# Performance work log

Hardware: AMD Instinct MI355X
Metric: run time of the kernel (lower is better)

Reference implementation:

```python
import jax, jax.numpy as jnp
import numpy as np

N, E, IN, D, G, C = 100000, 3200000, 128, 512, 64, 10
EPS = 1e-5

def _bn(x, g, b):
    # training-mode BatchNorm1d: batch statistics, biased variance
    m = jnp.mean(x, axis=0)
    v = jnp.var(x, axis=0)
    return (x - m) * jax.lax.rsqrt(v + EPS) * g + b

def _prelu(x, a):
    return jnp.where(x >= 0, x, a * x)

def setup_inputs() -> dict:
    key = jax.random.key(0)
    ks = jax.random.split(key, 16)
    def w(k, shape):
        fan_in = shape[0]
        s = 1.0 / np.sqrt(fan_in)
        return jax.random.uniform(k, shape, jnp.float32, -s, s)
    inp = {
        'x': jax.random.normal(ks[0], (N, IN), jnp.float32),
        'edge_index': jax.random.randint(ks[1], (2, E), 0, N),
        'batch': jnp.sort(jax.random.randint(ks[2], (N,), 0, G)),
        'bn1_g': jnp.ones((IN,), jnp.float32), 'bn1_b': jnp.zeros((IN,), jnp.float32),
        'w0': w(ks[3], (IN, D)), 'b0': jnp.zeros((D,), jnp.float32),
        'w1': w(ks[4], (D, D)), 'bb1': jnp.zeros((D,), jnp.float32),
        'w2': w(ks[5], (D, D)), 'bb2': jnp.zeros((D,), jnp.float32),
        'w3': w(ks[6], (D, D)), 'bb3': jnp.zeros((D,), jnp.float32),
        'bn3_g': jnp.ones((D,), jnp.float32), 'bn3_b': jnp.zeros((D,), jnp.float32),
        'a3': jnp.array([0.25], jnp.float32),
        'fc1_w': w(ks[7], (D, D)), 'fc1_b': jnp.zeros((D,), jnp.float32),
        'fc2_w': w(ks[8], (D, D // 2)), 'fc2_b': jnp.zeros((D // 2,), jnp.float32),
        'fc3_w': w(ks[9], (D // 2, C)), 'fc3_b': jnp.zeros((C,), jnp.float32),
    }
    return inp

def reference(x, edge_index, batch, bn1_g, bn1_b, w0, b0, w1, bb1, w2, bb2, w3, bb3,
              bn3_g, bn3_b, a3, fc1_w, fc1_b, fc2_w, fc2_b, fc3_w, fc3_b):
    # ChebConv with K=1 reduces to a plain linear layer (T_0(L)x = x); edge_index unused.
    h = _bn(x, bn1_g, bn1_b)
    h = jax.nn.relu(h @ w0 + b0)
    for w_, b_ in ((w1, bb1), (w2, bb2), (w3, bb3)):
        h = jax.nn.relu(h @ w_ + b_)
        h = _bn(h, bn3_g, bn3_b)   # same bn3 module reused each layer
    # global_add_pool: segment-sum of node features per graph
    h = jax.ops.segment_sum(h, batch, num_segments=G)
    h = _prelu(h @ fc1_w + fc1_b, a3)
    h = jax.nn.sigmoid(h @ fc2_w + fc2_b)
    return h @ fc3_w + fc3_b
```

## Files before the change

kernel.cpp:

```cpp
#include <hip/hip_runtime.h>
#include <math.h>

#define NN 100000
#define INF 128
#define DD  512
#define GG  64
#define CC  10

typedef __bf16 bf16;
typedef __bf16 bf16x8 __attribute__((ext_vector_type(8)));
typedef __bf16 bf16x4 __attribute__((ext_vector_type(4)));
typedef float  f32x4  __attribute__((ext_vector_type(4)));
typedef unsigned int u32x4 __attribute__((ext_vector_type(4)));


__global__ void zero_k(float* __restrict__ p, int n) {
    int i = blockIdx.x * blockDim.x + threadIdx.x;
    if (i < n) p[i] = 0.0f;
}

__global__ void bounds_k(const int* __restrict__ batch, int* __restrict__ starts) {
    int g = threadIdx.x;
    if (g <= GG) {
        int lo = 0, hi = NN;
        while (lo < hi) {
            int mid = (lo + hi) >> 1;
            if (batch[mid] < g) lo = mid + 1; else hi = mid;
        }
        starts[g] = lo;
    }
}

__global__ __launch_bounds__(256)
void colstats_cvt(const float* __restrict__ x, bf16* __restrict__ xb,
                  float* __restrict__ stats) {
    __shared__ float rs[4][128], rq[4][128];
    int t = threadIdx.x;
    int w = t >> 6, l = t & 63;
    int rg = t >> 5;
    int cq = t & 31;
    float s0 = 0, s1 = 0, s2 = 0, s3 = 0, q0 = 0, q1 = 0, q2 = 0, q3 = 0;
    for (int row = blockIdx.x * 8 + rg; row < NN; row += gridDim.x * 8) {
        float4 v = *(const float4*)&x[(size_t)row * INF + cq * 4];
        bf16x4 o; o[0] = (bf16)v.x; o[1] = (bf16)v.y; o[2] = (bf16)v.z; o[3] = (bf16)v.w;
        *(bf16x4*)&xb[(size_t)row * INF + cq * 4] = o;
        s0 += v.x; q0 += v.x * v.x;
        s1 += v.y; q1 += v.y * v.y;
        s2 += v.z; q2 += v.z * v.z;
        s3 += v.w; q3 += v.w * v.w;
    }
    s0 += __shfl_xor(s0, 32); s1 += __shfl_xor(s1, 32);
    s2 += __shfl_xor(s2, 32); s3 += __shfl_xor(s3, 32);
    q0 += __shfl_xor(q0, 32); q1 += __shfl_xor(q1, 32);
    q2 += __shfl_xor(q2, 32); q3 += __shfl_xor(q3, 32);
    if (l < 32) {
        rs[w][cq * 4 + 0] = s0; rs[w][cq * 4 + 1] = s1;
        rs[w][cq * 4 + 2] = s2; rs[w][cq * 4 + 3] = s3;
        rq[w][cq * 4 + 0] = q0; rq[w][cq * 4 + 1] = q1;
        rq[w][cq * 4 + 2] = q2; rq[w][cq * 4 + 3] = q3;
    }
    __syncthreads();
    if (t < 128) {
        atomicAdd(&stats[t],       rs[0][t] + rs[1][t] + rs[2][t] + rs[3][t]);
        atomicAdd(&stats[INF + t], rq[0][t] + rq[1][t] + rq[2][t] + rq[3][t]);
    }
}

__global__ void prep_st(const float* __restrict__ stats, int K,
                        const float* __restrict__ gamma, const float* __restrict__ beta,
                        float* __restrict__ s, float* __restrict__ t) {
    int j = blockIdx.x * blockDim.x + threadIdx.x;
    if (j < K) {
        const float invN = 1.0f / (float)NN;
        float mean = stats[j] * invN;
        float var  = stats[K + j] * invN - mean * mean;
        float sv   = gamma[j] * rsqrtf(var + 1e-5f);
        s[j] = sv;
        t[j] = beta[j] - mean * sv;
    }
}

__global__ __launch_bounds__(256)
void fold_wt(const float* __restrict__ s, const float* __restrict__ W,
             bf16* __restrict__ Wt, int K) {
    __shared__ float tile[64][68];
    __shared__ float sarr[64];
    int j0 = blockIdx.x * 64, k0 = blockIdx.y * 64;
    int t = threadIdx.x;
    if (t < 64) sarr[t] = s ? s[k0 + t] : 1.0f;
    int kk = t >> 2, jq = t & 3;
#pragma unroll
    for (int i = 0; i < 4; i++) {
        float4 v = *(const float4*)&W[(size_t)(k0 + kk) * DD + j0 + jq * 16 + i * 4];
        *(float4*)&tile[kk][jq * 16 + i * 4] = v;
    }
    __syncthreads();
    int jj = t >> 2, kq = t & 3;
    bf16 ov[16];
#pragma unroll
    for (int i = 0; i < 16; i++)
        ov[i] = (bf16)(tile[kq * 16 + i][jj] * sarr[kq * 16 + i]);
    bf16* dst = &Wt[(size_t)(j0 + jj) * K + k0 + kq * 16];
    *(u32x4*)dst       = *(u32x4*)&ov[0];
    *(u32x4*)(dst + 8) = *(u32x4*)&ov[8];
}

__global__ __launch_bounds__(256)
void fold_b(const float* __restrict__ tv, const float* __restrict__ W,
            const float* __restrict__ b, float* __restrict__ bp, int K) {
    __shared__ float red[4][64];
    int jj = threadIdx.x & 63, kr = threadIdx.x >> 6;
    int j = blockIdx.x * 64 + jj;
    float acc = 0.f;
    for (int k = kr; k < K; k += 4)
        acc += tv[k] * W[(size_t)k * DD + j];
    red[kr][jj] = acc;
    __syncthreads();
    if (kr == 0) bp[j] = b[j] + red[0][jj] + red[1][jj] + red[2][jj] + red[3][jj];
}

template <int K, int MODE>
__global__ __launch_bounds__(256, 2)
void gemm_mfma(const bf16* __restrict__ A, const bf16* __restrict__ Wt,
               const float* __restrict__ bias, bf16* __restrict__ H, int M,
               float* __restrict__ stats, const int* __restrict__ batch,
               float* __restrict__ R) {
    __shared__ bf16 smem[2 * 128 * 72];
    bf16* As = smem;
    bf16* Bs = smem + 128 * 72;
    const int t  = threadIdx.x;
    const int l  = t & 63;
    const int w  = t >> 6;
    const int wr = w >> 1, wc = w & 1;
    const int col0 = blockIdx.x * 128;
    const int row0 = blockIdx.y * 128;
    const int sr = t >> 1;
    const int sh = t & 1;

    f32x4 acc[4][4];
#pragma unroll
    for (int m = 0; m < 4; m++)
#pragma unroll
        for (int n = 0; n < 4; n++) acc[m][n] = (f32x4){0.f, 0.f, 0.f, 0.f};

    int ar = row0 + sr; if (ar >= M) ar = M - 1;
    const bf16* Asrc = A  + (size_t)ar * K + sh * 32;
    const bf16* Bsrc = Wt + (size_t)(col0 + sr) * K + sh * 32;

#pragma unroll 1
    for (int k0 = 0; k0 < K; k0 += 64) {
#pragma unroll
        for (int c = 0; c < 4; c++) {
            *(u32x4*)&As[sr * 72 + sh * 32 + c * 8] = *(const u32x4*)(Asrc + k0 + c * 8);
            *(u32x4*)&Bs[sr * 72 + sh * 32 + c * 8] = *(const u32x4*)(Bsrc + k0 + c * 8);
        }
        __syncthreads();
#pragma unroll
        for (int ks = 0; ks < 2; ks++) {
            bf16x8 af[4], bfr[4];
#pragma unroll
            for (int m = 0; m < 4; m++)
                af[m] = *(const bf16x8*)&As[(wr * 64 + m * 16 + (l & 15)) * 72 + ks * 32 + (l >> 4) * 8];
#pragma unroll
            for (int n = 0; n < 4; n++)
                bfr[n] = *(const bf16x8*)&Bs[(wc * 64 + n * 16 + (l & 15)) * 72 + ks * 32 + (l >> 4) * 8];
#pragma unroll
            for (int m = 0; m < 4; m++)
#pragma unroll
                for (int n = 0; n < 4; n++)
                    acc[m][n] = __builtin_amdgcn_mfma_f32_16x16x32_bf16(af[m], bfr[n], acc[m][n], 0, 0, 0);
        }
        __syncthreads();
    }

    float csumA[4], csqA[4];

    if (MODE <= 1) {
        bf16* ct = smem;
#pragma unroll
        for (int n = 0; n < 4; n++) {
            int lc = wc * 64 + n * 16 + (l & 15);
            float bv = bias[col0 + lc];
            float cs = 0.f, cq = 0.f;
#pragma unroll
            for (int m = 0; m < 4; m++) {
#pragma unroll
                for (int q = 0; q < 4; q++) {
                    int lr = wr * 64 + m * 16 + (l >> 4) * 4 + q;
                    float v = acc[m][n][q] + bv;
                    v = v > 0.f ? v : 0.f;
                    ct[lr * 136 + lc] = (bf16)v;
                    if (MODE == 1 && row0 + lr < M) { cs += v; cq += v * v; }
                }
            }
            csumA[n] = cs; csqA[n] = cq;
        }
        __syncthreads();
        {
            const char* cts = (const char*)ct;
            char* Hc = (char*)H;
#pragma unroll
            for (int i = 0; i < 8; i++) {
                int fo = i * 4096 + t * 16;
                int r  = fo >> 8;
                int cb = fo & 255;
                if (row0 + r < M)
                    *(u32x4*)(Hc + ((size_t)(row0 + r) * (DD * 2) + (size_t)col0 * 2 + cb)) =
                        *(const u32x4*)(cts + r * 272 + cb);
            }
        }
    } else {
        int gid[4][4];
#pragma unroll
        for (int m = 0; m < 4; m++)
#pragma unroll
            for (int q = 0; q < 4; q++) {
                int grow = row0 + wr * 64 + m * 16 + (l >> 4) * 4 + q;
                gid[m][q] = (grow < M) ? batch[grow] : -1;
            }
#pragma unroll
        for (int n = 0; n < 4; n++) {
            int col = col0 + wc * 64 + n * 16 + (l & 15);
            float bv = bias[col];
            float cs = 0.f, cq = 0.f;
            float ps = 0.f; int gc = -1;
#pragma unroll
            for (int m = 0; m < 4; m++) {
#pragma unroll
                for (int q = 0; q < 4; q++) {
                    int g = gid[m][q];
                    if (g >= 0) {
                        float v = acc[m][n][q] + bv;
                        v = v > 0.f ? v : 0.f;
                        cs += v; cq += v * v;
                        if (g != gc) {
                            if (gc >= 0) atomicAdd(&R[(size_t)gc * DD + col], ps);
                            ps = 0.f; gc = g;
                        }
                        ps += v;
                    }
                }
            }
            if (gc >= 0) atomicAdd(&R[(size_t)gc * DD + col], ps);
            csumA[n] = cs; csqA[n] = cq;
        }
    }

    if (MODE >= 1) {
#pragma unroll
        for (int n = 0; n < 4; n++) {
            float cs = csumA[n], cq = csqA[n];
            cs += __shfl_xor(cs, 16); cs += __shfl_xor(cs, 32);
            cq += __shfl_xor(cq, 16); cq += __shfl_xor(cq, 32);
            if ((l >> 4) == 0) {
                int col = col0 + wc * 64 + n * 16 + l;
                atomicAdd(&stats[col], cs);
                atomicAdd(&stats[DD + col], cq);
            }
        }
    }
}

__global__ __launch_bounds__(512)
void pool_fin(const float* __restrict__ R, const int* __restrict__ starts,
              const float* __restrict__ s4, const float* __restrict__ t4,
              float* __restrict__ P) {
    int g = blockIdx.x, j = threadIdx.x;
    float cnt = (float)(starts[g + 1] - starts[g]);
    P[g * DD + j] = R[(size_t)g * DD + j] * s4[j] + cnt * t4[j];
}

__global__ __launch_bounds__(256)
void head_k(const float* __restrict__ P,
            const float* __restrict__ fc1_w, const float* __restrict__ fc1_b,
            const float* __restrict__ fc2_w, const float* __restrict__ fc2_b,
            const float* __restrict__ fc3_w, const float* __restrict__ fc3_b,
            const float* __restrict__ a3, float* __restrict__ out) {
    __shared__ float p[DD], y1[DD], y2[DD / 2];
    int g = blockIdx.x, t = threadIdx.x;
    p[t]       = P[g * DD + t];
    p[t + 256] = P[g * DD + t + 256];
    __syncthreads();
    float alpha = a3[0];

    float acc0 = fc1_b[t], acc1 = fc1_b[t + 256];
    for (int k = 0; k < DD; k++) {
        float pv = p[k];
        acc0 = fmaf(pv, fc1_w[(size_t)k * DD + t], acc0);
        acc1 = fmaf(pv, fc1_w[(size_t)k * DD + t + 256], acc1);
    }
    y1[t]       = acc0 >= 0.f ? acc0 : alpha * acc0;
    y1[t + 256] = acc1 >= 0.f ? acc1 : alpha * acc1;
    __syncthreads();

    float acc = fc2_b[t];
    for (int k = 0; k < DD; k++) acc = fmaf(y1[k], fc2_w[(size_t)k * (DD / 2) + t], acc);
    y2[t] = 1.0f / (1.0f + expf(-acc));
    __syncthreads();

    if (t < CC) {
        float a = fc3_b[t];
        for (int k = 0; k < DD / 2; k++) a = fmaf(y2[k], fc3_w[(size_t)k * CC + t], a);
        out[g * CC + t] = a;
    }
}

extern "C" void kernel_launch(void* const* d_in, const int* in_sizes, int n_in,
                              void* d_out, int out_size, void* d_ws, size_t ws_size,
                              hipStream_t stream) {
    const float* x     = (const float*)d_in[0];
    const int*   batch = (const int*)d_in[2];
    const float* bn1_g = (const float*)d_in[3];
    const float* bn1_b = (const float*)d_in[4];
    const float* w0    = (const float*)d_in[5];
    const float* b0    = (const float*)d_in[6];
    const float* w1    = (const float*)d_in[7];
    const float* bb1   = (const float*)d_in[8];
    const float* w2    = (const float*)d_in[9];
    const float* bb2   = (const float*)d_in[10];
    const float* w3    = (const float*)d_in[11];
    const float* bb3   = (const float*)d_in[12];
    const float* bn3_g = (const float*)d_in[13];
    const float* bn3_b = (const float*)d_in[14];
    const float* a3    = (const float*)d_in[15];
    const float* fc1_w = (const float*)d_in[16];
    const float* fc1_b = (const float*)d_in[17];
    const float* fc2_w = (const float*)d_in[18];
    const float* fc2_b = (const float*)d_in[19];
    const float* fc3_w = (const float*)d_in[20];
    const float* fc3_b = (const float*)d_in[21];
    float* out = (float*)d_out;

    char* base = (char*)d_ws;
    const size_t HBYTES = (size_t)NN * DD * 2;
    bf16* Ha = (bf16*)base;
    bf16* Hb = (bf16*)(base + HBYTES);
    bf16* Xb = Hb;
    bf16* Wt = (bf16*)(base + 2 * HBYTES);
    float* f = (float*)(base + 2 * HBYTES + 524288);
    size_t off = 0;
    float* stats  = f + off; off += 3328;
    float* R      = f + off; off += (size_t)GG * DD;
    float* statsX = stats;
    float* stats2 = stats + 256;
    float* stats3 = stats + 1280;
    float* stats4 = stats + 2304;
    float* s1 = f + off; off += 128;
    float* t1 = f + off; off += 128;
    float* s2 = f + off; off += 512;
    float* t2 = f + off; off += 512;
    float* s3 = f + off; off += 512;
    float* t3 = f + off; off += 512;
    float* s4 = f + off; off += 512;
    float* t4 = f + off; off += 512;
    float* b0p = f + off; off += 512;
    float* bp  = f + off; off += 512;
    float* P   = f + off; off += (size_t)GG * DD;
    int*   starts = (int*)(f + off); off += 128;

    (void)in_sizes; (void)n_in; (void)out_size; (void)ws_size;

    const dim3 ggrid(4, (NN + 127) / 128);
    const int kZeroCount = 3328 + GG * DD;

    zero_k<<<(kZeroCount + 255) / 256, 256, 0, stream>>>(stats, kZeroCount);
    bounds_k<<<1, 128, 0, stream>>>(batch, starts);

    colstats_cvt<<<256, 256, 0, stream>>>(x, Xb, statsX);
    prep_st<<<1, 128, 0, stream>>>(statsX, 128, bn1_g, bn1_b, s1, t1);
    fold_wt<<<dim3(8, INF / 64), 256, 0, stream>>>(s1, w0, Wt, INF);
    fold_b<<<8, 256, 0, stream>>>(t1, w0, b0, b0p, INF);
    gemm_mfma<INF, 0><<<ggrid, 256, 0, stream>>>(Xb, Wt, b0p, Ha, NN, nullptr, nullptr, nullptr);

    fold_wt<<<dim3(8, DD / 64), 256, 0, stream>>>(nullptr, w1, Wt, DD);
    gemm_mfma<DD, 1><<<ggrid, 256, 0, stream>>>(Ha, Wt, bb1, Hb, NN, stats2, nullptr, nullptr);

    prep_st<<<2, 256, 0, stream>>>(stats2, 512, bn3_g, bn3_b, s2, t2);
    fold_wt<<<dim3(8, DD / 64), 256, 0, stream>>>(s2, w2, Wt, DD);
    fold_b<<<8, 256, 0, stream>>>(t2, w2, bb2, bp, DD);
    gemm_mfma<DD, 1><<<ggrid, 256, 0, stream>>>(Hb, Wt, bp, Ha, NN, stats3, nullptr, nullptr);

    prep_st<<<2, 256, 0, stream>>>(stats3, 512, bn3_g, bn3_b, s3, t3);
    fold_wt<<<dim3(8, DD / 64), 256, 0, stream>>>(s3, w3, Wt, DD);
    fold_b<<<8, 256, 0, stream>>>(t3, w3, bb3, bp, DD);
    gemm_mfma<DD, 2><<<ggrid, 256, 0, stream>>>(Ha, Wt, bp, nullptr, NN, stats4, batch, R);

    prep_st<<<2, 256, 0, stream>>>(stats4, 512, bn3_g, bn3_b, s4, t4);
    pool_fin<<<GG, 512, 0, stream>>>(R, starts, s4, t4, P);
    head_k<<<GG, 256, 0, stream>>>(P, fc1_w, fc1_b, fc2_w, fc2_b, fc3_w, fc3_b, a3, out);
}
```

Measured before the change: 639.1 us.

## Load GEMM tiles directly into LDS with XOR-swizzled layout

Replaces the register-staged global-to-shared copies in the MFMA GEMM with global_load_lds direct loads of 16 bytes per lane. The padded 72-stride shared layout becomes an unpadded 128-byte row layout with an XOR swizzle on the 16-byte slot, applied on both the load and fragment-read side, to avoid bank conflicts. Launch bounds are raised to 4 blocks per CU, which lowers the register budget per thread and risks spilling the 64-float accumulator. The smem buffer is kept at 18432 elements, presumably for the epilogue's reuse.

Result: faster. 605.5 us (-5.3%).

```diff
diff --git a/kernel.cpp b/kernel.cpp
--- a/kernel.cpp
+++ b/kernel.cpp
@@ -12,6 +12,12 @@
 typedef __bf16 bf16x4 __attribute__((ext_vector_type(4)));
 typedef float  f32x4  __attribute__((ext_vector_type(4)));
 typedef unsigned int u32x4 __attribute__((ext_vector_type(4)));
+
+__device__ __forceinline__ void gld16(const bf16* g, bf16* l) {
+    __builtin_amdgcn_global_load_lds(
+        (const __attribute__((address_space(1))) unsigned int*)g,
+        (__attribute__((address_space(3))) unsigned int*)l, 16, 0, 0);
+}
 
 
 __global__ void zero_k(float* __restrict__ p, int n) {
@@ -120,50 +126,58 @@
 }
 
 template <int K, int MODE>
-__global__ __launch_bounds__(256, 2)
+__global__ __launch_bounds__(256, 4)
 void gemm_mfma(const bf16* __restrict__ A, const bf16* __restrict__ Wt,
                const float* __restrict__ bias, bf16* __restrict__ H, int M,
                float* __restrict__ stats, const int* __restrict__ batch,
                float* __restrict__ R) {
-    __shared__ bf16 smem[2 * 128 * 72];
+    __shared__ bf16 smem[18432];
     bf16* As = smem;
-    bf16* Bs = smem + 128 * 72;
+    bf16* Bs = smem + 8192;
     const int t  = threadIdx.x;
     const int l  = t & 63;
     const int w  = t >> 6;
     const int wr = w >> 1, wc = w & 1;
     const int col0 = blockIdx.x * 128;
     const int row0 = blockIdx.y * 128;
-    const int sr = t >> 1;
-    const int sh = t & 1;
+
+    const int srow = w * 8 + (l >> 3);
+    const int sslt = l & 7;
 
     f32x4 acc[4][4];
 #pragma unroll
     for (int m = 0; m < 4; m++)
 #pragma unroll
         for (int n = 0; n < 4; n++) acc[m][n] = (f32x4){0.f, 0.f, 0.f, 0.f};
-
-    int ar = row0 + sr; if (ar >= M) ar = M - 1;
-    const bf16* Asrc = A  + (size_t)ar * K + sh * 32;
-    const bf16* Bsrc = Wt + (size_t)(col0 + sr) * K + sh * 32;
 
 #pragma unroll 1
     for (int k0 = 0; k0 < K; k0 += 64) {
 #pragma unroll
         for (int c = 0; c < 4; c++) {
-            *(u32x4*)&As[sr * 72 + sh * 32 + c * 8] = *(const u32x4*)(Asrc + k0 + c * 8);
-            *(u32x4*)&Bs[sr * 72 + sh * 32 + c * 8] = *(const u32x4*)(Bsrc + k0 + c * 8);
+            int r  = c * 32 + srow;
+            int sg = sslt ^ (r & 7);
+            int ga = row0 + r; if (ga >= M) ga = M - 1;
+            gld16(A  + (size_t)ga * K + k0 + sg * 8,
+                  (bf16*)((char*)As + c * 4096 + w * 1024));
+            gld16(Wt + (size_t)(col0 + r) * K + k0 + sg * 8,
+                  (bf16*)((char*)Bs + c * 4096 + w * 1024));
         }
         __syncthreads();
 #pragma unroll
         for (int ks = 0; ks < 2; ks++) {
             bf16x8 af[4], bfr[4];
 #pragma unroll
-            for (int m = 0; m < 4; m++)
-                af[m] = *(const bf16x8*)&As[(wr * 64 + m * 16 + (l & 15)) * 72 + ks * 32 + (l >> 4) * 8];
-#pragma unroll
-            for (int n = 0; n < 4; n++)
-                bfr[n] = *(const bf16x8*)&Bs[(wc * 64 + n * 16 + (l & 15)) * 72 + ks * 32 + (l >> 4) * 8];
+            for (int m = 0; m < 4; m++) {
+                int r = wr * 64 + m * 16 + (l & 15);
+                af[m] = *(const bf16x8*)((const char*)As + r * 128 +
+                        ((((ks << 2) + (l >> 4)) ^ (r & 7)) << 4));
+            }
+#pragma unroll
+            for (int n = 0; n < 4; n++) {
+                int r = wc * 64 + n * 16 + (l & 15);
+                bfr[n] = *(const bf16x8*)((const char*)Bs + r * 128 +
+                         ((((ks << 2) + (l >> 4)) ^ (r & 7)) << 4));
+            }
 #pragma unroll
             for (int m = 0; m < 4; m++)
 #pragma unroll
```
